# Kernel tuning notes

Hardware: AMD Instinct MI355X
Metric: run time of the kernel (lower is better)

Reference implementation:

```python
import jax, jax.numpy as jnp
import numpy as np

B, L, D = 32, 2048, 768
H = 512
EPS = 1e-5  # batch_norm eps (PyG MLP default norm)


def setup_inputs() -> dict:
    key = jax.random.key(0)
    ks = jax.random.split(key, 8)
    hidden = jax.random.normal(ks[0], (B, L, D), dtype=jnp.float32)
    attention_mask = jax.random.randint(ks[1], (B, L), 0, 2, dtype=jnp.int32)
    W1 = jax.random.normal(ks[2], (D, H), dtype=jnp.float32) * 0.02
    b1 = jnp.zeros((H,), dtype=jnp.float32)
    gamma = jnp.ones((H,), dtype=jnp.float32)
    beta = jnp.zeros((H,), dtype=jnp.float32)
    W2 = jax.random.normal(ks[3], (H, H), dtype=jnp.float32) * 0.02
    b2 = jnp.zeros((H,), dtype=jnp.float32)
    return {"hidden": hidden, "attention_mask": attention_mask,
            "W1": W1, "b1": b1, "gamma": gamma, "beta": beta,
            "W2": W2, "b2": b2}


def reference(hidden, attention_mask, W1, b1, gamma, beta, W2, b2):
    # Valid-token mask; pads are excluded from the batched graph's node set.
    m = attention_mask.astype(hidden.dtype)[..., None]  # (B, L, 1)
    n_valid = jnp.maximum(jnp.sum(m), 1.0)

    # MLP layer 1: Linear -> BatchNorm (stats over all valid nodes across the
    # whole batched graph, mirroring PyG MLP training-mode batch_norm) -> ReLU
    h = jnp.einsum('bld,dh->blh', hidden, W1) + b1  # (B, L, H)
    mean = jnp.sum(h * m, axis=(0, 1)) / n_valid
    var = jnp.sum(jnp.square(h - mean) * m, axis=(0, 1)) / n_valid
    h = (h - mean) * jax.lax.rsqrt(var + EPS) * gamma + beta
    h = jax.nn.relu(h)

    # MLP layer 2 (plain_last: no norm/act)
    out = jnp.einsum('blh,hk->blk', h, W2) + b2  # (B, L, H)

    # scores == ones -> segment softmax over each sequence's valid tokens is
    # uniform 1/n_b; scatter_add over batch ids == masked mean pool.
    counts = jnp.maximum(jnp.sum(m, axis=1), 1.0)  # (B, 1)
    pooled = jnp.sum(out * m, axis=1) / counts  # (B, H)
    return pooled
```

## Files before the change

### kernel.cpp

```cpp
#include <hip/hip_runtime.h>
#include <hip/hip_bf16.h>

#define Bn 32
#define Ln 2048
#define Dn 768
#define Hn 512
#define Mn (Bn*Ln)
#define EPSC 1e-5f

#define OFF_S1   0
#define OFF_S2   512
#define OFF_CNT  2048
#define OFF_PH   2304
#define OFF_W1T_BYTES  131072
#define OFF_H_BYTES    1048576

#define BM 128
#define BN2 256
#define BK 64
#define LDK 72
#define KT_N (Dn/BK)

typedef __attribute__((ext_vector_type(8))) short bf16x8;
typedef __attribute__((ext_vector_type(4))) float f32x4;

static __device__ __forceinline__ unsigned short f2bf(float x) {
  __hip_bfloat16 h = __float2bfloat16(x);
  return *reinterpret_cast<unsigned short*>(&h);
}
static __device__ __forceinline__ float bf2f(unsigned short u) {
  return __uint_as_float(((unsigned int)u) << 16);
}

__global__ __launch_bounds__(256) void pre_kernel(const int* __restrict__ mask,
                                                  float* __restrict__ ws) {
  int blk = blockIdx.x, t = threadIdx.x;
  if (blk < Bn) {
    __shared__ int red[256];
    int s = 0;
#pragma unroll
    for (int i = 0; i < 8; i++) s += mask[blk * Ln + i * 256 + t];
    red[t] = s;
    __syncthreads();
    for (int off = 128; off > 0; off >>= 1) {
      if (t < off) red[t] += red[t + off];
      __syncthreads();
    }
    if (t == 0) ws[OFF_CNT + blk] = (float)red[0];
  } else {
#pragma unroll
    for (int i = 0; i < 4; i++) ws[OFF_S1 + i * 256 + t] = 0.f;
#pragma unroll
    for (int i = 0; i < 64; i++) ws[OFF_PH + i * 256 + t] = 0.f;
  }
}

__global__ __launch_bounds__(256) void transpose_w1(
    const float* __restrict__ W1, unsigned short* __restrict__ W1t) {
  __shared__ float tile[32][33];
  int kx = blockIdx.x * 32;
  int nx = blockIdx.y * 32;
  int tx = threadIdx.x & 31, ty = threadIdx.x >> 5;
#pragma unroll
  for (int i = 0; i < 32; i += 8)
    tile[ty + i][tx] = W1[(size_t)(kx + ty + i) * Hn + nx + tx];
  __syncthreads();
#pragma unroll
  for (int i = 0; i < 32; i += 8)
    W1t[(size_t)(nx + ty + i) * Dn + kx + tx] = f2bf(tile[tx][ty + i]);
}

__global__ __launch_bounds__(512, 2) void gemm1_mfma(
    const float* __restrict__ A, const unsigned short* __restrict__ W1t,
    const float* __restrict__ b1, const int* __restrict__ mask,
    unsigned short* __restrict__ Hout,
    float* __restrict__ gsum, float* __restrict__ gsq)
{
  __shared__ __align__(16) unsigned short As3[2][BM * LDK];
  __shared__ __align__(16) unsigned short Bs3[2][BN2 * BK];
  __shared__ float csum[BN2];
  __shared__ float csq[BN2];

  const int t = threadIdx.x;
  const int bx = blockIdx.x;
  const int by = blockIdx.y;
  const int bm0 = by * BM;
  const int bn0 = bx * BN2;

  const int w = t >> 6;
  const int lane = t & 63;
  const int wm0 = (w >> 2) * 64;
  const int wn0 = (w & 3) * 64;
  const int l15 = lane & 15;
  const int quad = lane >> 4;

  const int am = t >> 2;
  const int ak = (t & 3) * 16;
  const float* Ap = A + (size_t)(bm0 + am) * Dn + ak;

  f32x4 acc[4][4];
#pragma unroll
  for (int i = 0; i < 4; i++)
#pragma unroll
    for (int j = 0; j < 4; j++) acc[i][j] = (f32x4){0.f, 0.f, 0.f, 0.f};

  float4 rAe[4], rAo[4];

#define WAITV(N) do { asm volatile("s_waitcnt vmcnt(" #N ")" ::: "memory"); \
                      __builtin_amdgcn_sched_barrier(0); } while (0)
#define WAITL0() do { asm volatile("s_waitcnt lgkmcnt(0)" ::: "memory"); \
                      __builtin_amdgcn_sched_barrier(0); } while (0)

#define STAGE_B(KT2, NS) do { \
  _Pragma("unroll") \
  for (int j = 0; j < 4; ++j) { \
    const int p = ((w * 4 + j) << 10) + (lane << 4); \
    const int q = p ^ (((p >> 7) & 7) << 4); \
    const char* gsrc = (const char*)(W1t + (size_t)(bn0 + (q >> 7)) * Dn \
                                     + (KT2) * BK) + (q & 127); \
    __builtin_amdgcn_global_load_lds( \
        (const __attribute__((address_space(1))) void*)gsrc, \
        (__attribute__((address_space(3))) void*)((char*)&Bs3[NS][0] \
                                                  + ((w * 4 + j) << 10)), \
        16, 0, 0); \
  } \
} while (0)

#define LOAD_A(KT, R) do { \
  R[0] = *(const float4*)(Ap + (KT) * BK); \
  R[1] = *(const float4*)(Ap + (KT) * BK + 4); \
  R[2] = *(const float4*)(Ap + (KT) * BK + 8); \
  R[3] = *(const float4*)(Ap + (KT) * BK + 12); \
} while (0)

#define PACK_WRITE(R, NS) do { \
  uint4 p0, p1; \
  p0.x = (unsigned)f2bf(R[0].x) | ((unsigned)f2bf(R[0].y) << 16); \
  p0.y = (unsigned)f2bf(R[0].z) | ((unsigned)f2bf(R[0].w) << 16); \
  p0.z = (unsigned)f2bf(R[1].x) | ((unsigned)f2bf(R[1].y) << 16); \
  p0.w = (unsigned)f2bf(R[1].z) | ((unsigned)f2bf(R[1].w) << 16); \
  p1.x = (unsigned)f2bf(R[2].x) | ((unsigned)f2bf(R[2].y) << 16); \
  p1.y = (unsigned)f2bf(R[2].z) | ((unsigned)f2bf(R[2].w) << 16); \
  p1.z = (unsigned)f2bf(R[3].x) | ((unsigned)f2bf(R[3].y) << 16); \
  p1.w = (unsigned)f2bf(R[3].z) | ((unsigned)f2bf(R[3].w) << 16); \
  *(uint4*)&As3[NS][am * LDK + ak] = p0; \
  *(uint4*)&As3[NS][am * LDK + ak + 8] = p1; \
} while (0)

#define MFMA_ALL(CS) do { \
  _Pragma("unroll") \
  for (int s = 0; s < 2; ++s) { \
    bf16x8 af[4], bf[4]; \
    _Pragma("unroll") \
    for (int mt = 0; mt < 4; ++mt) \
      af[mt] = *(const bf16x8*)&As3[CS][(wm0 + mt * 16 + l15) * LDK \
                                        + s * 32 + quad * 8]; \
    _Pragma("unroll") \
    for (int nt = 0; nt < 4; ++nt) { \
      const int rb = wn0 + nt * 16 + l15; \
      const int cb = (s * 64 + quad * 16) ^ ((rb & 7) << 4); \
      bf[nt] = *(const bf16x8*)((const char*)&Bs3[CS][0] + rb * 128 + cb); \
    } \
    _Pragma("unroll") \
    for (int mt = 0; mt < 4; ++mt) \
      _Pragma("unroll") \
      for (int nt = 0; nt < 4; ++nt) \
        acc[mt][nt] = __builtin_amdgcn_mfma_f32_16x16x32_bf16( \
            af[mt], bf[nt], acc[mt][nt], 0, 0, 0); \
  } \
} while (0)

#define K_ITER(KT, CS, RL, RW) do { \
  if ((KT) < KT_N - 1) STAGE_B((KT) + 1, (CS) ^ 1); \
  __builtin_amdgcn_sched_barrier(0); \
  if ((KT) < KT_N - 2) LOAD_A((KT) + 2, RL); \
  if ((KT) < KT_N - 1) PACK_WRITE(RW, (CS) ^ 1); \
  MFMA_ALL(CS); \
  if ((KT) < KT_N - 2) { WAITV(4); } else { WAITV(0); } \
  WAITL0(); \
  __builtin_amdgcn_s_barrier(); \
} while (0)

  STAGE_B(0, 0);
  __builtin_amdgcn_sched_barrier(0);
  LOAD_A(0, rAe);
  LOAD_A(1, rAo);
  WAITV(0);
  PACK_WRITE(rAe, 0);
  WAITL0();
  __builtin_amdgcn_s_barrier();

#pragma unroll
  for (int k2 = 0; k2 < KT_N / 2; ++k2) {
    K_ITER(k2 * 2,     0, rAe, rAo);
    K_ITER(k2 * 2 + 1, 1, rAo, rAe);
  }

#undef K_ITER
#undef MFMA_ALL
#undef PACK_WRITE
#undef LOAD_A
#undef STAGE_B
#undef WAITL0
#undef WAITV

  if (t < BN2) { csum[t] = 0.f; csq[t] = 0.f; }
  __syncthreads();

  float mk[4][4];
#pragma unroll
  for (int mt = 0; mt < 4; mt++) {
    int4 mv = *(const int4*)(mask + bm0 + wm0 + mt * 16 + quad * 4);
    mk[mt][0] = (float)mv.x; mk[mt][1] = (float)mv.y;
    mk[mt][2] = (float)mv.z; mk[mt][3] = (float)mv.w;
  }

  const size_t cbase = ((size_t)(by * 2 + bx)) * 32768 + (size_t)w * 4096;
#pragma unroll
  for (int nt = 0; nt < 4; nt++) {
    const int nl = wn0 + nt * 16 + l15;
    const float bias = b1[bn0 + nl];
    float ps = 0.f, pq = 0.f;
#pragma unroll
    for (int mt = 0; mt < 4; mt++) {
      ushort4 st;
      float v0 = acc[mt][nt][0] + bias;
      float v1 = acc[mt][nt][1] + bias;
      float v2 = acc[mt][nt][2] + bias;
      float v3 = acc[mt][nt][3] + bias;
      ps += v0 * mk[mt][0] + v1 * mk[mt][1] + v2 * mk[mt][2] + v3 * mk[mt][3];
      pq += v0 * v0 * mk[mt][0] + v1 * v1 * mk[mt][1] +
            v2 * v2 * mk[mt][2] + v3 * v3 * mk[mt][3];
      st.x = f2bf(v0); st.y = f2bf(v1); st.z = f2bf(v2); st.w = f2bf(v3);
      *(ushort4*)&Hout[cbase + (size_t)(mt * 4 + nt) * 256 + lane * 4] = st;
    }
    atomicAdd(&csum[nl], ps);
    atomicAdd(&csq[nl], pq);
  }

  __syncthreads();
  if (t < BN2) {
    atomicAdd(&gsum[bn0 + t], csum[t]);
    atomicAdd(&gsq[bn0 + t], csq[t]);
  }
}

__global__ __launch_bounds__(256) void bnpool_kernel(
    const unsigned short* __restrict__ Hbuf, const int* __restrict__ mask,
    const float* __restrict__ ws, const float* __restrict__ gamma,
    const float* __restrict__ beta, float* __restrict__ PH)
{
  __shared__ float mkf[BM];
  __shared__ float redc[32];
  const int t = threadIdx.x;
  const int chunk = blockIdx.x;
  const int by = chunk >> 1, bx = chunk & 1;
  const int b = chunk >> 5;
  if (t < 32) redc[t] = ws[OFF_CNT + t];
  if (t < BM) mkf[t] = (float)mask[by * BM + t];
  __syncthreads();

  float nv = 0.f;
#pragma unroll
  for (int i = 0; i < 32; i++) nv += redc[i];
  nv = fmaxf(nv, 1.f);
  const float inv = 1.f / nv;
  const int c = bx * BN2 + t;
  const float m = ws[OFF_S1 + c] * inv;
  const float var = ws[OFF_S2 + c] * inv - m * m;
  const float istd = rsqrtf(fmaxf(var, 0.f) + EPSC);
  const float scv = istd * gamma[c];
  const float shv = beta[c] - m * scv;

  const int w3 = t >> 6, nt = (t >> 4) & 3, l15 = t & 15;
  float acc = 0.f;
#pragma unroll
  for (int h = 0; h < 2; h++) {
    const int w = w3 + h * 4;
    const int wm0 = h * 64;
    const unsigned short* base =
        Hbuf + (size_t)chunk * 32768 + (size_t)w * 4096 + nt * 256 + l15 * 4;
#pragma unroll
    for (int mt = 0; mt < 4; mt++)
#pragma unroll
      for (int q = 0; q < 4; q++) {
        ushort4 hv = *(const ushort4*)(base + mt * 1024 + q * 64);
        const float* mv = &mkf[wm0 + mt * 16 + q * 4];
        acc += fmaxf(fmaf(bf2f(hv.x), scv, shv), 0.f) * mv[0]
             + fmaxf(fmaf(bf2f(hv.y), scv, shv), 0.f) * mv[1]
             + fmaxf(fmaf(bf2f(hv.z), scv, shv), 0.f) * mv[2]
             + fmaxf(fmaf(bf2f(hv.w), scv, shv), 0.f) * mv[3];
      }
  }
  atomicAdd(&PH[b * Hn + c], acc);
}

__global__ __launch_bounds__(128) void final_kernel(
    const float* __restrict__ pooledh, const float* __restrict__ cnt,
    const float* __restrict__ W2, const float* __restrict__ b2,
    float* __restrict__ out)
{
  __shared__ float pr[Hn];
  int b = blockIdx.x >> 2;
  int cc = blockIdx.x & 3;
  int t = threadIdx.x;
  float nb = cnt[b];
  float inv = 1.f / fmaxf(nb, 1.f);
#pragma unroll
  for (int i = 0; i < 4; i++)
    pr[t + i * 128] = pooledh[b * Hn + t + i * 128] * inv;
  __syncthreads();
  int c = cc * 128 + t;
  float a0 = 0.f, a1 = 0.f, a2 = 0.f, a3 = 0.f;
  for (int i = 0; i < Hn; i += 4) {
    a0 = fmaf(pr[i],     W2[(size_t)i * Hn + c],       a0);
    a1 = fmaf(pr[i + 1], W2[(size_t)(i + 1) * Hn + c], a1);
    a2 = fmaf(pr[i + 2], W2[(size_t)(i + 2) * Hn + c], a2);
    a3 = fmaf(pr[i + 3], W2[(size_t)(i + 3) * Hn + c], a3);
  }
  out[b * Hn + c] = (a0 + a1) + (a2 + a3) + b2[c] * (nb * inv);
}

extern "C" void kernel_launch(void* const* d_in, const int* in_sizes, int n_in,
                              void* d_out, int out_size, void* d_ws, size_t ws_size,
                              hipStream_t stream) {
  const float* hidden = (const float*)d_in[0];
  const int*   mask   = (const int*)d_in[1];
  const float* W1     = (const float*)d_in[2];
  const float* b1     = (const float*)d_in[3];
  const float* gamma  = (const float*)d_in[4];
  const float* beta   = (const float*)d_in[5];
  const float* W2     = (const float*)d_in[6];
  const float* b2     = (const float*)d_in[7];
  float* out = (float*)d_out;
  float* ws  = (float*)d_ws;
  unsigned short* W1t  = (unsigned short*)((char*)d_ws + OFF_W1T_BYTES);
  unsigned short* Hbuf = (unsigned short*)((char*)d_ws + OFF_H_BYTES);

  pre_kernel<<<Bn + 1, 256, 0, stream>>>(mask, ws);
  transpose_w1<<<dim3(Dn / 32, Hn / 32), 256, 0, stream>>>(W1, W1t);
  gemm1_mfma<<<dim3(Hn / BN2, Mn / BM), 512, 0, stream>>>(
      hidden, W1t, b1, mask, Hbuf, ws + OFF_S1, ws + OFF_S2);
  bnpool_kernel<<<(Mn / BM) * (Hn / BN2), 256, 0, stream>>>(
      Hbuf, mask, ws, gamma, beta, ws + OFF_PH);
  final_kernel<<<Bn * 4, 128, 0, stream>>>(ws + OFF_PH, ws + OFF_CNT, W2, b2, out);
}
```

Baseline: 392.7 us.

## Single-buffer swizzled A tile in LDS to fit more gemm1 blocks per CU

The padded double-buffered A tile becomes a single XOR-swizzled bf16 buffer. The column-stat scratch arrays now alias that buffer after the K loop. This cuts LDS use per block so more blocks can be resident, and launch bounds are raised from 2 to 4 blocks per CU. To make the single buffer safe, each K iteration adds a second barrier before the packed A write, and the tighter register budget from the new launch bounds may cause spills of the 64-float accumulator.

After: 448.5 us. +14.2%, slower.

```diff
diff --git a/kernel.cpp b/kernel.cpp
--- a/kernel.cpp
+++ b/kernel.cpp
@@ -18,7 +18,6 @@
 #define BM 128
 #define BN2 256
 #define BK 64
-#define LDK 72
 #define KT_N (Dn/BK)
 
 typedef __attribute__((ext_vector_type(8))) short bf16x8;
@@ -70,16 +69,14 @@
     W1t[(size_t)(nx + ty + i) * Dn + kx + tx] = f2bf(tile[tx][ty + i]);
 }
 
-__global__ __launch_bounds__(512, 2) void gemm1_mfma(
+__global__ __launch_bounds__(512, 4) void gemm1_mfma(
     const float* __restrict__ A, const unsigned short* __restrict__ W1t,
     const float* __restrict__ b1, const int* __restrict__ mask,
     unsigned short* __restrict__ Hout,
     float* __restrict__ gsum, float* __restrict__ gsq)
 {
-  __shared__ __align__(16) unsigned short As3[2][BM * LDK];
-  __shared__ __align__(16) unsigned short Bs3[2][BN2 * BK];
-  __shared__ float csum[BN2];
-  __shared__ float csq[BN2];
+  __shared__ __align__(16) unsigned short As[BM * BK];
+  __shared__ __align__(16) unsigned short Bs[2][BN2 * BK];
 
   const int t = threadIdx.x;
   const int bx = blockIdx.x;
@@ -97,6 +94,9 @@
   const int am = t >> 2;
   const int ak = (t & 3) * 16;
   const float* Ap = A + (size_t)(bm0 + am) * Dn + ak;
+  const int aswz = (am & 7) << 4;
+  const int ab0 = am * 128 + ((ak * 2) ^ aswz);
+  const int ab1 = am * 128 + ((ak * 2 + 16) ^ aswz);
 
   f32x4 acc[4][4];
 #pragma unroll
@@ -120,7 +120,7 @@
                                      + (KT2) * BK) + (q & 127); \
     __builtin_amdgcn_global_load_lds( \
         (const __attribute__((address_space(1))) void*)gsrc, \
-        (__attribute__((address_space(3))) void*)((char*)&Bs3[NS][0] \
+        (__attribute__((address_space(3))) void*)((char*)&Bs[NS][0] \
                                                   + ((w * 4 + j) << 10)), \
         16, 0, 0); \
   } \
@@ -133,7 +133,7 @@
   R[3] = *(const float4*)(Ap + (KT) * BK + 12); \
 } while (0)
 
-#define PACK_WRITE(R, NS) do { \
+#define PACK_WRITE(R) do { \
   uint4 p0, p1; \
   p0.x = (unsigned)f2bf(R[0].x) | ((unsigned)f2bf(R[0].y) << 16); \
   p0.y = (unsigned)f2bf(R[0].z) | ((unsigned)f2bf(R[0].w) << 16); \
@@ -143,8 +143,8 @@
   p1.y = (unsigned)f2bf(R[2].z) | ((unsigned)f2bf(R[2].w) << 16); \
   p1.z = (unsigned)f2bf(R[3].x) | ((unsigned)f2bf(R[3].y) << 16); \
   p1.w = (unsigned)f2bf(R[3].z) | ((unsigned)f2bf(R[3].w) << 16); \
-  *(uint4*)&As3[NS][am * LDK + ak] = p0; \
-  *(uint4*)&As3[NS][am * LDK + ak + 8] = p1; \
+  *(uint4*)((char*)&As[0] + ab0) = p0; \
+  *(uint4*)((char*)&As[0] + ab1) = p1; \
 } while (0)
 
 #define MFMA_ALL(CS) do { \
@@ -152,14 +152,16 @@
   for (int s = 0; s < 2; ++s) { \
     bf16x8 af[4], bf[4]; \
     _Pragma("unroll") \
-    for (int mt = 0; mt < 4; ++mt) \
-      af[mt] = *(const bf16x8*)&As3[CS][(wm0 + mt * 16 + l15) * LDK \
-                                        + s * 32 + quad * 8]; \
+    for (int mt = 0; mt < 4; ++mt) { \
+      const int ra = wm0 + mt * 16 + l15; \
+      const int ca = (s * 64 + quad * 16) ^ ((ra & 7) << 4); \
+      af[mt] = *(const bf16x8*)((const char*)&As[0] + ra * 128 + ca); \
+    } \
     _Pragma("unroll") \
     for (int nt = 0; nt < 4; ++nt) { \
       const int rb = wn0 + nt * 16 + l15; \
       const int cb = (s * 64 + quad * 16) ^ ((rb & 7) << 4); \
-      bf[nt] = *(const bf16x8*)((const char*)&Bs3[CS][0] + rb * 128 + cb); \
+      bf[nt] = *(const bf16x8*)((const char*)&Bs[CS][0] + rb * 128 + cb); \
     } \
     _Pragma("unroll") \
     for (int mt = 0; mt < 4; ++mt) \
@@ -170,30 +172,31 @@
   } \
 } while (0)
 
-#define K_ITER(KT, CS, RL, RW) do { \
+#define K_ITER(KT, CS, RNEXT, RLOAD) do { \
   if ((KT) < KT_N - 1) STAGE_B((KT) + 1, (CS) ^ 1); \
   __builtin_amdgcn_sched_barrier(0); \
-  if ((KT) < KT_N - 2) LOAD_A((KT) + 2, RL); \
-  if ((KT) < KT_N - 1) PACK_WRITE(RW, (CS) ^ 1); \
+  if ((KT) < KT_N - 2) LOAD_A((KT) + 2, RLOAD); \
   MFMA_ALL(CS); \
   if ((KT) < KT_N - 2) { WAITV(4); } else { WAITV(0); } \
+  __builtin_amdgcn_s_barrier();             \
+  if ((KT) < KT_N - 1) { PACK_WRITE(RNEXT); } \
   WAITL0(); \
-  __builtin_amdgcn_s_barrier(); \
+  __builtin_amdgcn_s_barrier();             \
 } while (0)
 
   STAGE_B(0, 0);
   __builtin_amdgcn_sched_barrier(0);
   LOAD_A(0, rAe);
   LOAD_A(1, rAo);
+  PACK_WRITE(rAe);
   WAITV(0);
-  PACK_WRITE(rAe, 0);
   WAITL0();
   __builtin_amdgcn_s_barrier();
 
 #pragma unroll
   for (int k2 = 0; k2 < KT_N / 2; ++k2) {
-    K_ITER(k2 * 2,     0, rAe, rAo);
-    K_ITER(k2 * 2 + 1, 1, rAo, rAe);
+    K_ITER(k2 * 2,     0, rAo, rAe);
+    K_ITER(k2 * 2 + 1, 1, rAe, rAo);
   }
 
 #undef K_ITER
@@ -204,6 +207,8 @@
 #undef WAITL0
 #undef WAITV
 
+  float* csum = (float*)&As[0];
+  float* csq  = csum + BN2;
   if (t < BN2) { csum[t] = 0.f; csq[t] = 0.f; }
   __syncthreads();
 
```
